# Kernel tuning notes

Measured on AMD Instinct MI355X. Metric: run time of the kernel, lower is better.

## Reference

```python
import jax, jax.numpy as jnp
import numpy as np

N = 50000
E = 800000
IN_DIM = 256
OUT_DIM = 128
HEADS = 4
D_K = OUT_DIM // HEADS  # 32
BETA = 1.0  # beta_init, requires_grad=False (constant)
NEG_SLOPE = 0.2
EPS = 1e-12


def setup_inputs() -> dict:
    key = jax.random.key(0)
    k = jax.random.split(key, 8)
    H = jax.random.normal(k[0], (N, IN_DIM), dtype=jnp.float32)
    edge_index = jax.random.randint(k[1], (2, E), 0, N, dtype=jnp.int64)
    sim1_edge = jax.random.normal(k[2], (E,), dtype=jnp.float32)
    # Parameters (torch nn.Linear stores weight as (out, in); y = x @ W.T)
    W = jax.random.normal(k[3], (HEADS * D_K, IN_DIM), dtype=jnp.float32) * (1.0 / np.sqrt(IN_DIM))
    a_src = jax.random.normal(k[4], (HEADS, D_K), dtype=jnp.float32)
    a_dst = jax.random.normal(k[5], (HEADS, D_K), dtype=jnp.float32)
    msg_lin_w = jax.random.normal(k[6], (D_K, D_K), dtype=jnp.float32) * (1.0 / np.sqrt(D_K))
    return {"H": H, "edge_index": edge_index, "sim1_edge": sim1_edge,
            "W": W, "a_src": a_src, "a_dst": a_dst, "msg_lin_w": msg_lin_w}


def reference(H, edge_index, sim1_edge, W, a_src, a_dst, msg_lin_w):
    n = H.shape[0]
    H_proj = (H @ W.T).reshape(n, HEADS, D_K)           # [N, h, d_k]
    src, dst = edge_index[0], edge_index[1]
    h_src = H_proj[src]                                  # [E, h, d_k]
    h_dst = H_proj[dst]                                  # [E, h, d_k]
    # per-edge attention logits (struct + semantic)
    e = (jnp.einsum('ehd,hd->eh', h_src, a_src)
         + jnp.einsum('ehd,hd->eh', h_dst, a_dst)
         + BETA * sim1_edge[:, None])                    # [E, h]
    e = jnp.where(e >= 0, e, NEG_SLOPE * e)              # LeakyReLU(0.2)
    # global (per-head) max for stabilization, matching original e.max(dim=0)
    e = e - jnp.max(e, axis=0, keepdims=True)
    exp_e = jnp.exp(e)                                   # [E, h]
    denom = jax.ops.segment_sum(exp_e, dst, num_segments=n)  # [N, h]
    alpha = exp_e / (denom[dst] + EPS)                   # [E, h]  (dropout p=0 -> identity)
    m = alpha[:, :, None] * h_src                        # [E, h, d_k]
    out = jax.ops.segment_sum(m, dst, num_segments=n)    # [N, h, d_k]
    out_h = out.reshape(n, HEADS * D_K)                  # concat=True
    msg_base = jnp.einsum('ehd,od->eho', h_src, msg_lin_w).mean(axis=1)  # [E, d_k]
    alpha_mean = alpha.mean(axis=1)                      # [E]
    return out_h, alpha_mean, msg_base
```

## Files before the change

kernel.cpp:

```cpp
#include <hip/hip_runtime.h>
#include <hip/hip_bf16.h>
#include <float.h>

#define HEADS 4
#define DK 32

static constexpr float kBeta = 1.0f;
static constexpr float kNeg  = 0.2f;
static constexpr float kEps  = 1e-12f;

__device__ __forceinline__ float bf2f(unsigned short v) {
  return __uint_as_float((unsigned)v << 16);
}
__device__ __forceinline__ float2 bfp2(unsigned u) {
  return make_float2(__uint_as_float(u << 16), __uint_as_float(u & 0xFFFF0000u));
}
__device__ __forceinline__ unsigned fkey(float x) {
  unsigned u = __float_as_uint(x);
  return (u & 0x80000000u) ? ~u : (u | 0x80000000u);
}
__device__ __forceinline__ float funkey(unsigned k) {
  unsigned u = (k & 0x80000000u) ? (k & 0x7fffffffu) : ~k;
  return __uint_as_float(u);
}

__global__ __launch_bounds__(256) void k_detect_edges(const int* __restrict__ ei32,
                                                      int* __restrict__ eflag, int E) {
  int i = blockIdx.x * 256 + threadIdx.x;
  if (2 * i + 1 < 2 * E && ei32[2 * i + 1] != 0) atomicOr(eflag, 1);
}

__global__ __launch_bounds__(256) void k_detect_dtype(const unsigned* __restrict__ Hw,
                                                      int* __restrict__ dflag, int nw) {
  int i = blockIdx.x * 256 + threadIdx.x;
  if (i < nw && ((Hw[i] >> 7) & 0xFFu) == 0xFFu) atomicOr(dflag, 1);
}

__global__ __launch_bounds__(256) void k_cvt(const int* __restrict__ ei32,
                                             const int* __restrict__ eflag,
                                             int* __restrict__ src_i,
                                             int* __restrict__ dst_i,
                                             int* __restrict__ deg, int E) {
  int i = blockIdx.x * 256 + threadIdx.x;
  if (i >= E) return;
  int s, d;
  if (*eflag) { s = ei32[i];     d = ei32[E + i]; }
  else        { s = ei32[2 * i]; d = ei32[2 * E + 2 * i]; }
  src_i[i] = s;
  dst_i[i] = d;
  atomicAdd(deg + d, 1);
}

__global__ __launch_bounds__(256) void k_f32cvt(const void* __restrict__ in,
                                                float* __restrict__ out,
                                                const int* __restrict__ dflag, int n) {
  int i = blockIdx.x * 256 + threadIdx.x;
  if (i >= n) return;
  out[i] = (*dflag) ? ((const float*)in)[i] : bf2f(((const unsigned short*)in)[i]);
}

__global__ __launch_bounds__(256) void k_wcvt(const void* __restrict__ in,
                                              float* __restrict__ out,
                                              const int* __restrict__ dflag, int n) {
  int i = blockIdx.x * 256 + threadIdx.x;
  if (i >= n) return;
  int r = i >> 8, c = i & 255;
  float v = (*dflag) ? ((const float*)in)[i] : bf2f(((const unsigned short*)in)[i]);
  out[(size_t)c * 128 + r] = v;
}

__global__ __launch_bounds__(256) void k_scan1(const int* __restrict__ deg,
                                               int* __restrict__ bsum, int N) {
  const int t = threadIdx.x;
  int i = blockIdx.x * 256 + t;
  int v = (i < N) ? deg[i] : 0;
#pragma unroll
  for (int off = 32; off; off >>= 1) v += __shfl_xor(v, off);
  __shared__ int red[4];
  if ((t & 63) == 0) red[t >> 6] = v;
  __syncthreads();
  if (t == 0) bsum[blockIdx.x] = red[0] + red[1] + red[2] + red[3];
}
__global__ __launch_bounds__(1024) void k_scan2(int* __restrict__ bsum, int nb) {
  __shared__ int part[1024];
  const int t = threadIdx.x;
  part[t] = (t < nb) ? bsum[t] : 0;
  __syncthreads();
  int own = part[t];
  for (int off = 1; off < 1024; off <<= 1) {
    int v = (t >= off) ? part[t - off] : 0;
    __syncthreads();
    part[t] += v;
    __syncthreads();
  }
  if (t < nb) bsum[t] = part[t] - own;
}
__global__ __launch_bounds__(256) void k_scan3(const int* __restrict__ deg,
                                               const int* __restrict__ bsum,
                                               int* __restrict__ row_ptr,
                                               int* __restrict__ cursor, int N) {
  __shared__ int part[256];
  const int t = threadIdx.x;
  int i = blockIdx.x * 256 + t;
  int v = (i < N) ? deg[i] : 0;
  part[t] = v;
  __syncthreads();
  for (int off = 1; off < 256; off <<= 1) {
    int x = (t >= off) ? part[t - off] : 0;
    __syncthreads();
    part[t] += x;
    __syncthreads();
  }
  int excl = part[t] - v + bsum[blockIdx.x];
  if (i < N) {
    row_ptr[i] = excl;
    cursor[i]  = excl;
    if (i == N - 1) row_ptr[N] = excl + v;
  }
}

__global__ __launch_bounds__(256) void k_fill(const int* __restrict__ dst,
                                              int* __restrict__ cursor,
                                              int* __restrict__ eidx, int E) {
  int e = blockIdx.x * 256 + threadIdx.x;
  if (e >= E) return;
  int pos = atomicAdd(cursor + dst[e], 1);
  eidx[pos] = e;
}

__global__ __launch_bounds__(256) void k_proj(const void* __restrict__ Hraw,
                                              const float* __restrict__ Wtf,
                                              const int* __restrict__ dflag,
                                              float* __restrict__ Hproj, int N) {
  __shared__ float Ht[32][260];
  const int t = threadIdx.x;
  const int nb = blockIdx.x * 32;
  const int dt = *dflag;
  if (dt) {
    const float4* __restrict__ H4 = (const float4*)Hraw;
#pragma unroll
    for (int i = 0; i < 8; ++i) {
      int f = t + i * 256;
      int r = f >> 6, kq = f & 63;
      float4 v = make_float4(0.f, 0.f, 0.f, 0.f);
      if (nb + r < N) v = H4[(size_t)(nb + r) * 64 + kq];
      *(float4*)&Ht[r][4 * kq] = v;
    }
  } else {
    const uint4* __restrict__ H8 = (const uint4*)Hraw;
#pragma unroll
    for (int i = 0; i < 4; ++i) {
      int g = t + i * 256;
      int r = g >> 5, c8 = g & 31;
      uint4 v = make_uint4(0u, 0u, 0u, 0u);
      if (nb + r < N) v = H8[(size_t)(nb + r) * 32 + c8];
      float2 f0 = bfp2(v.x), f1 = bfp2(v.y), f2 = bfp2(v.z), f3 = bfp2(v.w);
      *(float4*)&Ht[r][c8 * 8 + 0] = make_float4(f0.x, f0.y, f1.x, f1.y);
      *(float4*)&Ht[r][c8 * 8 + 4] = make_float4(f2.x, f2.y, f3.x, f3.y);
    }
  }
  __syncthreads();
  const int cg = (t & 31);
  const int n0 = (t >> 5) * 4;
  float acc[4][4];
#pragma unroll
  for (int n = 0; n < 4; ++n)
#pragma unroll
    for (int j = 0; j < 4; ++j) acc[n][j] = 0.f;
  const float4* __restrict__ Wt4 = (const float4*)Wtf;
#pragma unroll 4
  for (int kk = 0; kk < 256; kk += 4) {
    float4 w0 = Wt4[(size_t)(kk + 0) * 32 + cg];
    float4 w1 = Wt4[(size_t)(kk + 1) * 32 + cg];
    float4 w2 = Wt4[(size_t)(kk + 2) * 32 + cg];
    float4 w3 = Wt4[(size_t)(kk + 3) * 32 + cg];
#pragma unroll
    for (int n = 0; n < 4; ++n) {
      float4 h = *(const float4*)&Ht[n0 + n][kk];
      acc[n][0] += h.x * w0.x + h.y * w1.x + h.z * w2.x + h.w * w3.x;
      acc[n][1] += h.x * w0.y + h.y * w1.y + h.z * w2.y + h.w * w3.y;
      acc[n][2] += h.x * w0.z + h.y * w1.z + h.z * w2.z + h.w * w3.z;
      acc[n][3] += h.x * w0.w + h.y * w1.w + h.z * w2.w + h.w * w3.w;
    }
  }
#pragma unroll
  for (int n = 0; n < 4; ++n) {
    int row = nb + n0 + n;
    if (row < N)
      *(float4*)&Hproj[(size_t)row * 128 + 4 * cg] =
          make_float4(acc[n][0], acc[n][1], acc[n][2], acc[n][3]);
  }
}

__global__ __launch_bounds__(256) void k_node(const float* __restrict__ Hproj,
                                              const float* __restrict__ af,
                                              const float* __restrict__ msgwf,
                                              float* __restrict__ s_src,
                                              float* __restrict__ s_dst,
                                              float* __restrict__ msgb, int N) {
  const int l = threadIdx.x & 63;
  const int wb = threadIdx.x >> 6;
  const int n = (blockIdx.x << 2) + wb;
  if (n >= N) return;
  const float* row = Hproj + (size_t)n * 128;
  float h0 = row[l], h1 = row[64 + l];
  float p0 = h0 * af[l],       p1 = h1 * af[64 + l];
  float q0 = h0 * af[128 + l], q1 = h1 * af[192 + l];
#pragma unroll
  for (int off = 16; off; off >>= 1) {
    p0 += __shfl_xor(p0, off);
    p1 += __shfl_xor(p1, off);
    q0 += __shfl_xor(q0, off);
    q1 += __shfl_xor(q1, off);
  }
  if (l == 0)  { s_src[n*4+0] = p0; s_src[n*4+2] = p1; s_dst[n*4+0] = q0; s_dst[n*4+2] = q1; }
  if (l == 32) { s_src[n*4+1] = p0; s_src[n*4+3] = p1; s_dst[n*4+1] = q0; s_dst[n*4+3] = q1; }
  float t4 = h0 + __shfl_xor(h0, 32) + h1 + __shfl_xor(h1, 32);
  float hbar = 0.25f * t4;
  if (l < DK) {
    float acc = 0.f;
#pragma unroll
    for (int d = 0; d < DK; ++d) acc += __shfl(hbar, d) * msgwf[l * DK + d];
    msgb[(size_t)n * DK + l] = acc;
  }
}

__global__ __launch_bounds__(256) void k_logits(const int* __restrict__ src,
                                                const int* __restrict__ dst,
                                                const void* __restrict__ sim1,
                                                const int* __restrict__ dflag,
                                                const float* __restrict__ s_src,
                                                const float* __restrict__ s_dst,
                                                float4* __restrict__ e_vals,
                                                unsigned* __restrict__ gmax, int E) {
  const int e = blockIdx.x * 256 + threadIdx.x;
  float m0 = -FLT_MAX, m1 = -FLT_MAX, m2 = -FLT_MAX, m3 = -FLT_MAX;
  if (e < E) {
    int s = src[e], d = dst[e];
    float4 ss = *(const float4*)(s_src + (size_t)s * 4);
    float4 sd = *(const float4*)(s_dst + (size_t)d * 4);
    float sv = (*dflag) ? ((const float*)sim1)[e] : bf2f(((const unsigned short*)sim1)[e]);
    float b = kBeta * sv;
    float e0 = ss.x + sd.x + b; e0 = (e0 >= 0.f) ? e0 : kNeg * e0;
    float e1 = ss.y + sd.y + b; e1 = (e1 >= 0.f) ? e1 : kNeg * e1;
    float e2 = ss.z + sd.z + b; e2 = (e2 >= 0.f) ? e2 : kNeg * e2;
    float e3 = ss.w + sd.w + b; e3 = (e3 >= 0.f) ? e3 : kNeg * e3;
    e_vals[e] = make_float4(e0, e1, e2, e3);
    m0 = e0; m1 = e1; m2 = e2; m3 = e3;
  }
#pragma unroll
  for (int off = 32; off; off >>= 1) {
    m0 = fmaxf(m0, __shfl_xor(m0, off));
    m1 = fmaxf(m1, __shfl_xor(m1, off));
    m2 = fmaxf(m2, __shfl_xor(m2, off));
    m3 = fmaxf(m3, __shfl_xor(m3, off));
  }
  __shared__ float red[4][4];
  if ((threadIdx.x & 63) == 0) {
    int w = threadIdx.x >> 6;
    red[w][0] = m0; red[w][1] = m1; red[w][2] = m2; red[w][3] = m3;
  }
  __syncthreads();
  if (threadIdx.x < 4) {
    int h = threadIdx.x;
    float mm = fmaxf(fmaxf(red[0][h], red[1][h]), fmaxf(red[2][h], red[3][h]));
    atomicMax(gmax + h, fkey(mm));
  }
}

__global__ __launch_bounds__(256) void k_msg(const int* __restrict__ src,
                                             const float* __restrict__ msgb,
                                             const int* __restrict__ dflag,
                                             void* __restrict__ d_out,
                                             int N, int E) {
  long long tid = (long long)blockIdx.x * 256 + threadIdx.x;
  if (tid >= (long long)E * DK) return;
  int e = (int)(tid >> 5), j = (int)(tid & 31);
  float mv = msgb[(size_t)src[e] * DK + j];
  const size_t msg_off = (size_t)N * 128 + (size_t)E;
  if (*dflag) ((float*)d_out)[msg_off + (size_t)e * DK + j] = mv;
  else        ((__hip_bfloat16*)d_out)[msg_off + (size_t)e * DK + j] = __float2bfloat16(mv);
}

__global__ __launch_bounds__(256) void k_out(const int* __restrict__ row_ptr,
                                             const int* __restrict__ eidx,
                                             const int* __restrict__ src,
                                             const float4* __restrict__ e_vals,
                                             const unsigned* __restrict__ gmax,
                                             const float* __restrict__ Hproj,
                                             const int* __restrict__ dflag,
                                             void* __restrict__ d_out, int N, int E) {
  const int n = (int)((blockIdx.x * 256 + threadIdx.x) >> 6);
  const int l = threadIdx.x & 63;
  if (n >= N) return;
  const int beg = row_ptr[n];
  const int deg = row_ptr[n + 1] - beg;
  const int dt = *dflag;
  const float m0 = funkey(gmax[0]), m1 = funkey(gmax[1]);
  const float m2 = funkey(gmax[2]), m3 = funkey(gmax[3]);
  const size_t alpha_off = (size_t)N * 128;
  float acc_lo = 0.f, acc_hi = 0.f;
  float4 dn = make_float4(0.f, 0.f, 0.f, 0.f);
  int eid = 0, s = 0;
  float4 ev = make_float4(0.f, 0.f, 0.f, 0.f);
  const bool small = (deg <= 64);
  if (small) {
    if (l < deg) {
      eid = eidx[beg + l];
      float4 r = e_vals[eid];
      ev = make_float4(expf(r.x - m0), expf(r.y - m1),
                       expf(r.z - m2), expf(r.w - m3));
      s = src[eid];
      dn = ev;
    }
  } else {
    for (int base = 0; base < deg; base += 64) {
      if (base + l < deg) {
        int e2 = eidx[beg + base + l];
        float4 r = e_vals[e2];
        dn.x += expf(r.x - m0); dn.y += expf(r.y - m1);
        dn.z += expf(r.z - m2); dn.w += expf(r.w - m3);
      }
    }
  }
#pragma unroll
  for (int off = 32; off; off >>= 1) {
    dn.x += __shfl_xor(dn.x, off);
    dn.y += __shfl_xor(dn.y, off);
    dn.z += __shfl_xor(dn.z, off);
    dn.w += __shfl_xor(dn.w, off);
  }
  const float i0 = 1.f / (dn.x + kEps), i1 = 1.f / (dn.y + kEps);
  const float i2 = 1.f / (dn.z + kEps), i3 = 1.f / (dn.w + kEps);
  if (small) {
    if (l < deg) {
      float am = 0.25f * (ev.x * i0 + ev.y * i1 + ev.z * i2 + ev.w * i3);
      if (dt) ((float*)d_out)[alpha_off + eid] = am;
      else    ((__hip_bfloat16*)d_out)[alpha_off + eid] = __float2bfloat16(am);
    }
    for (int i = 0; i < deg; ++i) {
      int si = __shfl(s, i);
      float ax = __shfl(ev.x, i), ay = __shfl(ev.y, i);
      float az = __shfl(ev.z, i), aw = __shfl(ev.w, i);
      float a_lo = (l < 32) ? ax * i0 : ay * i1;
      float a_hi = (l < 32) ? az * i2 : aw * i3;
      acc_lo += a_lo * Hproj[(size_t)si * 128 + l];
      acc_hi += a_hi * Hproj[(size_t)si * 128 + 64 + l];
    }
  } else {
    for (int base = 0; base < deg; base += 64) {
      int cnt = min(64, deg - base);
      int eid2 = 0, s2 = 0;
      float4 e2 = make_float4(0.f, 0.f, 0.f, 0.f);
      if (l < cnt) {
        eid2 = eidx[beg + base + l];
        float4 r = e_vals[eid2];
        e2 = make_float4(expf(r.x - m0), expf(r.y - m1),
                         expf(r.z - m2), expf(r.w - m3));
        s2 = src[eid2];
        float am = 0.25f * (e2.x * i0 + e2.y * i1 + e2.z * i2 + e2.w * i3);
        if (dt) ((float*)d_out)[alpha_off + eid2] = am;
        else    ((__hip_bfloat16*)d_out)[alpha_off + eid2] = __float2bfloat16(am);
      }
      for (int i = 0; i < cnt; ++i) {
        int si = __shfl(s2, i);
        float ax = __shfl(e2.x, i), ay = __shfl(e2.y, i);
        float az = __shfl(e2.z, i), aw = __shfl(e2.w, i);
        float a_lo = (l < 32) ? ax * i0 : ay * i1;
        float a_hi = (l < 32) ? az * i2 : aw * i3;
        acc_lo += a_lo * Hproj[(size_t)si * 128 + l];
        acc_hi += a_hi * Hproj[(size_t)si * 128 + 64 + l];
      }
    }
  }
  if (dt) {
    ((float*)d_out)[(size_t)n * 128 + l]      = acc_lo;
    ((float*)d_out)[(size_t)n * 128 + 64 + l] = acc_hi;
  } else {
    ((__hip_bfloat16*)d_out)[(size_t)n * 128 + l]      = __float2bfloat16(acc_lo);
    ((__hip_bfloat16*)d_out)[(size_t)n * 128 + 64 + l] = __float2bfloat16(acc_hi);
  }
}

extern "C" void kernel_launch(void* const* d_in, const int* in_sizes, int n_in,
                              void* d_out, int out_size, void* d_ws, size_t ws_size,
                              hipStream_t stream) {
  const void* H     = d_in[0];
  const int*  ei    = (const int*)d_in[1];
  const void* sim1  = d_in[2];
  const void* W     = d_in[3];
  const void* a_src = d_in[4];
  const void* a_dst = d_in[5];
  const void* msg_w = d_in[6];
  const int N = in_sizes[0] / 256;
  const int E = in_sizes[2];
  const int NB = (N + 255) / 256;

  float* ws      = (float*)d_ws;
  float* Hproj   = ws;
  float* s_src   = Hproj  + (size_t)N * 128;
  float* s_dst   = s_src  + (size_t)N * 4;
  float* msgb    = s_dst  + (size_t)N * 4;
  float* e_vals  = msgb   + (size_t)N * 32;
  int* deg       = (int*)(e_vals + (size_t)E * 4);
  unsigned* gmax = (unsigned*)(deg + N);
  int* eflag     = (int*)(gmax + 4);
  int* dflag     = eflag + 1;
  int* row_ptr   = dflag + 1;
  int* cursor    = row_ptr + N + 1;
  int* bsum      = cursor + N;
  int* eidx      = bsum + 1024;
  int* src_i     = eidx + E;
  int* dst_i     = src_i + E;
  float* Wtf     = (float*)(dst_i + E);
  float* af      = Wtf + 128 * 256;
  float* msgwf   = af + 256;

  hipMemsetAsync(deg, 0, (size_t)(N + 6) * sizeof(int), stream);

  k_detect_edges<<<16, 256, 0, stream>>>(ei, eflag, E);
  k_detect_dtype<<<512, 256, 0, stream>>>((const unsigned*)H, dflag, 131072);
  k_cvt<<<(E + 255) / 256, 256, 0, stream>>>(ei, eflag, src_i, dst_i, deg, E);
  k_wcvt<<<128, 256, 0, stream>>>(W, Wtf, dflag, 128 * 256);
  k_f32cvt<<<1, 256, 0, stream>>>(a_src, af, dflag, 128);
  k_f32cvt<<<1, 256, 0, stream>>>(a_dst, af + 128, dflag, 128);
  k_f32cvt<<<4, 256, 0, stream>>>(msg_w, msgwf, dflag, 1024);
  k_proj<<<(N + 31) / 32, 256, 0, stream>>>(H, Wtf, dflag, Hproj, N);
  k_scan1<<<NB, 256, 0, stream>>>(deg, bsum, N);
  k_scan2<<<1, 1024, 0, stream>>>(bsum, NB);
  k_scan3<<<NB, 256, 0, stream>>>(deg, bsum, row_ptr, cursor, N);
  k_fill<<<(E + 255) / 256, 256, 0, stream>>>(dst_i, cursor, eidx, E);
  k_node<<<(N + 3) / 4, 256, 0, stream>>>(Hproj, af, msgwf, s_src, s_dst, msgb, N);
  k_logits<<<(E + 255) / 256, 256, 0, stream>>>(src_i, dst_i, sim1, dflag, s_src, s_dst,
                                                (float4*)e_vals, gmax, E);
  k_msg<<<(int)(((long long)E * DK + 255) / 256), 256, 0, stream>>>(src_i, msgb, dflag,
                                                                    d_out, N, E);
  k_out<<<(int)(((size_t)N * 64 + 255) / 256), 256, 0, stream>>>(
      row_ptr, eidx, src_i, (const float4*)e_vals, gmax, Hproj, dflag, d_out, N, E);
}
```

Measured before the change: 544.2 us.

## Store gather operands in fp16, recompute edge logits in aggregation, merge setup kernels

Hproj and the message base are now also written as fp16 copies. The aggregation and message kernels gather these half-size rows, with each lane handling a packed half2 pair and writing vectorized outputs. The per-edge logit buffer is no longer stored: the aggregation kernel recomputes the logits from s_src, s_dst and sim1, which removes an E×16-byte write and read. Small detect and parameter conversion kernels are merged into fewer launches, at the cost of fp16 rounding error in gathered features and message outputs.

After: 515.1 us. 1.06x faster.

```diff
diff --git a/kernel.cpp b/kernel.cpp
--- a/kernel.cpp
+++ b/kernel.cpp
@@ -1,5 +1,6 @@
 #include <hip/hip_runtime.h>
 #include <hip/hip_bf16.h>
+#include <hip/hip_fp16.h>
 #include <float.h>
 
 #define HEADS 4
@@ -24,15 +25,13 @@
   return __uint_as_float(u);
 }
 
-__global__ __launch_bounds__(256) void k_detect_edges(const int* __restrict__ ei32,
-                                                      int* __restrict__ eflag, int E) {
+__global__ __launch_bounds__(256) void k_detect(const int* __restrict__ ei32,
+                                                const unsigned* __restrict__ Hw,
+                                                int* __restrict__ eflag,
+                                                int* __restrict__ dflag,
+                                                int E, int nw) {
   int i = blockIdx.x * 256 + threadIdx.x;
-  if (2 * i + 1 < 2 * E && ei32[2 * i + 1] != 0) atomicOr(eflag, 1);
-}
-
-__global__ __launch_bounds__(256) void k_detect_dtype(const unsigned* __restrict__ Hw,
-                                                      int* __restrict__ dflag, int nw) {
-  int i = blockIdx.x * 256 + threadIdx.x;
+  if (i < 4096 && 2 * i + 1 < 2 * E && ei32[2 * i + 1] != 0) atomicOr(eflag, 1);
   if (i < nw && ((Hw[i] >> 7) & 0xFFu) == 0xFFu) atomicOr(dflag, 1);
 }
 
@@ -51,12 +50,23 @@
   atomicAdd(deg + d, 1);
 }
 
-__global__ __launch_bounds__(256) void k_f32cvt(const void* __restrict__ in,
-                                                float* __restrict__ out,
-                                                const int* __restrict__ dflag, int n) {
+__global__ __launch_bounds__(256) void k_params(const void* __restrict__ a_src,
+                                                const void* __restrict__ a_dst,
+                                                const void* __restrict__ msg_w,
+                                                float* __restrict__ af,
+                                                float* __restrict__ msgwf,
+                                                const int* __restrict__ dflag) {
   int i = blockIdx.x * 256 + threadIdx.x;
-  if (i >= n) return;
-  out[i] = (*dflag) ? ((const float*)in)[i] : bf2f(((const unsigned short*)in)[i]);
+  int dt = *dflag;
+  if (i < 128) {
+    af[i] = dt ? ((const float*)a_src)[i] : bf2f(((const unsigned short*)a_src)[i]);
+  } else if (i < 256) {
+    int j = i - 128;
+    af[i] = dt ? ((const float*)a_dst)[j] : bf2f(((const unsigned short*)a_dst)[j]);
+  } else if (i < 1280) {
+    int j = i - 256;
+    msgwf[j] = dt ? ((const float*)msg_w)[j] : bf2f(((const unsigned short*)msg_w)[j]);
+  }
 }
 
 __global__ __launch_bounds__(256) void k_wcvt(const void* __restrict__ in,
@@ -197,13 +207,16 @@
                                               const float* __restrict__ msgwf,
                                               float* __restrict__ s_src,
                                               float* __restrict__ s_dst,
-                                              float* __restrict__ msgb, int N) {
+                                              __half* __restrict__ msgb,
+                                              __half* __restrict__ Hb, int N) {
   const int l = threadIdx.x & 63;
   const int wb = threadIdx.x >> 6;
   const int n = (blockIdx.x << 2) + wb;
   if (n >= N) return;
   const float* row = Hproj + (size_t)n * 128;
   float h0 = row[l], h1 = row[64 + l];
+  Hb[(size_t)n * 128 + l]      = __float2half(h0);
+  Hb[(size_t)n * 128 + 64 + l] = __float2half(h1);
   float p0 = h0 * af[l],       p1 = h1 * af[64 + l];
   float q0 = h0 * af[128 + l], q1 = h1 * af[192 + l];
 #pragma unroll
@@ -221,7 +234,7 @@
     float acc = 0.f;
 #pragma unroll
     for (int d = 0; d < DK; ++d) acc += __shfl(hbar, d) * msgwf[l * DK + d];
-    msgb[(size_t)n * DK + l] = acc;
+    msgb[(size_t)n * DK + l] = __float2half(acc);
   }
 }
 
@@ -231,7 +244,6 @@
                                                 const int* __restrict__ dflag,
                                                 const float* __restrict__ s_src,
                                                 const float* __restrict__ s_dst,
-                                                float4* __restrict__ e_vals,
                                                 unsigned* __restrict__ gmax, int E) {
   const int e = blockIdx.x * 256 + threadIdx.x;
   float m0 = -FLT_MAX, m1 = -FLT_MAX, m2 = -FLT_MAX, m3 = -FLT_MAX;
@@ -245,7 +257,6 @@
     float e1 = ss.y + sd.y + b; e1 = (e1 >= 0.f) ? e1 : kNeg * e1;
     float e2 = ss.z + sd.z + b; e2 = (e2 >= 0.f) ? e2 : kNeg * e2;
     float e3 = ss.w + sd.w + b; e3 = (e3 >= 0.f) ? e3 : kNeg * e3;
-    e_vals[e] = make_float4(e0, e1, e2, e3);
     m0 = e0; m1 = e1; m2 = e2; m3 = e3;
   }
 #pragma unroll
@@ -269,25 +280,32 @@
 }
 
 __global__ __launch_bounds__(256) void k_msg(const int* __restrict__ src,
-                                             const float* __restrict__ msgb,
+                                             const __half2* __restrict__ msgb2,
                                              const int* __restrict__ dflag,
                                              void* __restrict__ d_out,
                                              int N, int E) {
   long long tid = (long long)blockIdx.x * 256 + threadIdx.x;
-  if (tid >= (long long)E * DK) return;
-  int e = (int)(tid >> 5), j = (int)(tid & 31);
-  float mv = msgb[(size_t)src[e] * DK + j];
+  if (tid >= (long long)E * 16) return;
+  int e = (int)(tid >> 4), jp = (int)(tid & 15);
+  __half2 hv = msgb2[(size_t)src[e] * 16 + jp];
+  float2 f = __half22float2(hv);
   const size_t msg_off = (size_t)N * 128 + (size_t)E;
-  if (*dflag) ((float*)d_out)[msg_off + (size_t)e * DK + j] = mv;
-  else        ((__hip_bfloat16*)d_out)[msg_off + (size_t)e * DK + j] = __float2bfloat16(mv);
+  if (*dflag) {
+    *(float2*)&((float*)d_out)[msg_off + (size_t)e * 32 + 2 * jp] = f;
+  } else {
+    __hip_bfloat162 b = __float22bfloat162_rn(f);
+    *(__hip_bfloat162*)((__hip_bfloat16*)d_out + msg_off + (size_t)e * 32 + 2 * jp) = b;
+  }
 }
 
 __global__ __launch_bounds__(256) void k_out(const int* __restrict__ row_ptr,
                                              const int* __restrict__ eidx,
                                              const int* __restrict__ src,
-                                             const float4* __restrict__ e_vals,
+                                             const void* __restrict__ sim1,
+                                             const float* __restrict__ s_src,
+                                             const float* __restrict__ s_dst,
                                              const unsigned* __restrict__ gmax,
-                                             const float* __restrict__ Hproj,
+                                             const unsigned* __restrict__ Hb_u,
                                              const int* __restrict__ dflag,
                                              void* __restrict__ d_out, int N, int E) {
   const int n = (int)((blockIdx.x * 256 + threadIdx.x) >> 6);
@@ -298,8 +316,9 @@
   const int dt = *dflag;
   const float m0 = funkey(gmax[0]), m1 = funkey(gmax[1]);
   const float m2 = funkey(gmax[2]), m3 = funkey(gmax[3]);
+  const float4 sd = *(const float4*)(s_dst + (size_t)n * 4);
   const size_t alpha_off = (size_t)N * 128;
-  float acc_lo = 0.f, acc_hi = 0.f;
+  float accx = 0.f, accy = 0.f;
   float4 dn = make_float4(0.f, 0.f, 0.f, 0.f);
   int eid = 0, s = 0;
   float4 ev = make_float4(0.f, 0.f, 0.f, 0.f);
@@ -307,19 +326,29 @@
   if (small) {
     if (l < deg) {
       eid = eidx[beg + l];
-      float4 r = e_vals[eid];
-      ev = make_float4(expf(r.x - m0), expf(r.y - m1),
-                       expf(r.z - m2), expf(r.w - m3));
       s = src[eid];
+      float4 ss = *(const float4*)(s_src + (size_t)s * 4);
+      float sv = dt ? ((const float*)sim1)[eid] : bf2f(((const unsigned short*)sim1)[eid]);
+      float e0 = ss.x + sd.x + sv; e0 = (e0 >= 0.f) ? e0 : kNeg * e0;
+      float e1 = ss.y + sd.y + sv; e1 = (e1 >= 0.f) ? e1 : kNeg * e1;
+      float e2 = ss.z + sd.z + sv; e2 = (e2 >= 0.f) ? e2 : kNeg * e2;
+      float e3 = ss.w + sd.w + sv; e3 = (e3 >= 0.f) ? e3 : kNeg * e3;
+      ev = make_float4(expf(e0 - m0), expf(e1 - m1), expf(e2 - m2), expf(e3 - m3));
       dn = ev;
     }
   } else {
     for (int base = 0; base < deg; base += 64) {
       if (base + l < deg) {
-        int e2 = eidx[beg + base + l];
-        float4 r = e_vals[e2];
-        dn.x += expf(r.x - m0); dn.y += expf(r.y - m1);
-        dn.z += expf(r.z - m2); dn.w += expf(r.w - m3);
+        int e2i = eidx[beg + base + l];
+        int s2 = src[e2i];
+        float4 ss = *(const float4*)(s_src + (size_t)s2 * 4);
+        float sv = dt ? ((const float*)sim1)[e2i] : bf2f(((const unsigned short*)sim1)[e2i]);
+        float e0 = ss.x + sd.x + sv; e0 = (e0 >= 0.f) ? e0 : kNeg * e0;
+        float e1 = ss.y + sd.y + sv; e1 = (e1 >= 0.f) ? e1 : kNeg * e1;
+        float e2 = ss.z + sd.z + sv; e2 = (e2 >= 0.f) ? e2 : kNeg * e2;
+        float e3 = ss.w + sd.w + sv; e3 = (e3 >= 0.f) ? e3 : kNeg * e3;
+        dn.x += expf(e0 - m0); dn.y += expf(e1 - m1);
+        dn.z += expf(e2 - m2); dn.w += expf(e3 - m3);
       }
     }
   }
@@ -332,6 +361,7 @@
   }
   const float i0 = 1.f / (dn.x + kEps), i1 = 1.f / (dn.y + kEps);
   const float i2 = 1.f / (dn.z + kEps), i3 = 1.f / (dn.w + kEps);
+  const float myinv = (l < 32) ? ((l < 16) ? i0 : i1) : ((l < 48) ? i2 : i3);
   if (small) {
     if (l < deg) {
       float am = 0.25f * (ev.x * i0 + ev.y * i1 + ev.z * i2 + ev.w * i3);
@@ -342,43 +372,48 @@
       int si = __shfl(s, i);
       float ax = __shfl(ev.x, i), ay = __shfl(ev.y, i);
       float az = __shfl(ev.z, i), aw = __shfl(ev.w, i);
-      float a_lo = (l < 32) ? ax * i0 : ay * i1;
-      float a_hi = (l < 32) ? az * i2 : aw * i3;
-      acc_lo += a_lo * Hproj[(size_t)si * 128 + l];
-      acc_hi += a_hi * Hproj[(size_t)si * 128 + 64 + l];
+      float aa = ((l < 32) ? ((l < 16) ? ax : ay) : ((l < 48) ? az : aw)) * myinv;
+      unsigned u = Hb_u[(size_t)si * 64 + l];
+      float2 f = __half22float2(*(const __half2*)&u);
+      accx += aa * f.x;
+      accy += aa * f.y;
     }
   } else {
     for (int base = 0; base < deg; base += 64) {
       int cnt = min(64, deg - base);
       int eid2 = 0, s2 = 0;
-      float4 e2 = make_float4(0.f, 0.f, 0.f, 0.f);
+      float4 e2v = make_float4(0.f, 0.f, 0.f, 0.f);
       if (l < cnt) {
         eid2 = eidx[beg + base + l];
-        float4 r = e_vals[eid2];
-        e2 = make_float4(expf(r.x - m0), expf(r.y - m1),
-                         expf(r.z - m2), expf(r.w - m3));
         s2 = src[eid2];
-        float am = 0.25f * (e2.x * i0 + e2.y * i1 + e2.z * i2 + e2.w * i3);
+        float4 ss = *(const float4*)(s_src + (size_t)s2 * 4);
+        float sv = dt ? ((const float*)sim1)[eid2] : bf2f(((const unsigned short*)sim1)[eid2]);
+        float e0 = ss.x + sd.x + sv; e0 = (e0 >= 0.f) ? e0 : kNeg * e0;
+        float e1 = ss.y + sd.y + sv; e1 = (e1 >= 0.f) ? e1 : kNeg * e1;
+        float e2 = ss.z + sd.z + sv; e2 = (e2 >= 0.f) ? e2 : kNeg * e2;
+        float e3 = ss.w + sd.w + sv; e3 = (e3 >= 0.f) ? e3 : kNeg * e3;
+        e2v = make_float4(expf(e0 - m0), expf(e1 - m1), expf(e2 - m2), expf(e3 - m3));
+        float am = 0.25f * (e2v.x * i0 + e2v.y * i1 + e2v.z * i2 + e2v.w * i3);
         if (dt) ((float*)d_out)[alpha_off + eid2] = am;
         else    ((__hip_bfloat16*)d_out)[alpha_off + eid2] = __float2bfloat16(am);
       }
       for (int i = 0; i < cnt; ++i) {
         int si = __shfl(s2, i);
-        float ax = __shfl(e2.x, i), ay = __shfl(e2.y, i);
-        float az = __shfl(e2.z, i), aw = __shfl(e2.w, i);
-        float a_lo = (l < 32) ? ax * i0 : ay * i1;
-        float a_hi = (l < 32) ? az * i2 : aw * i3;
-        acc_lo += a_lo * Hproj[(size_t)si * 128 + l];
-        acc_hi += a_hi * Hproj[(size_t)si * 128 + 64 + l];
+        float ax = __shfl(e2v.x, i), ay = __shfl(e2v.y, i);
+        float az = __shfl(e2v.z, i), aw = __shfl(e2v.w, i);
+        float aa = ((l < 32) ? ((l < 16) ? ax : ay) : ((l < 48) ? az : aw)) * myinv;
+        unsigned u = Hb_u[(size_t)si * 64 + l];
+        float2 f = __half22float2(*(const __half2*)&u);
+        accx += aa * f.x;
+        accy += aa * f.y;
       }
     }
   }
   if (dt) {
-    ((float*)d_out)[(size_t)n * 128 + l]      = acc_lo;
-    ((float*)d_out)[(size_t)n * 128 + 64 + l] = acc_hi;
+    *(float2*)&((float*)d_out)[(size_t)n * 128 + 2 * l] = make_float2(accx, accy);
   } else {
-    ((__hip_bfloat16*)d_out)[(size_t)n * 128 + l]      = __float2bfloat16(acc_lo);
-    ((__hip_bfloat16*)d_out)[(size_t)n * 128 + 64 + l] = __float2bfloat16(acc_hi);
+    __hip_bfloat162 b = __float22bfloat162_rn(make_float2(accx, accy));
+    *(__hip_bfloat162*)((__hip_bfloat16*)d_out + (size_t)n * 128 + 2 * l) = b;
   }
 }
 
@@ -396,45 +431,43 @@
   const int E = in_sizes[2];
   const int NB = (N + 255) / 256;
 
-  float* ws      = (float*)d_ws;
-  float* Hproj   = ws;
-  float* s_src   = Hproj  + (size_t)N * 128;
-  float* s_dst   = s_src  + (size_t)N * 4;
-  float* msgb    = s_dst  + (size_t)N * 4;
-  float* e_vals  = msgb   + (size_t)N * 32;
-  int* deg       = (int*)(e_vals + (size_t)E * 4);
-  unsigned* gmax = (unsigned*)(deg + N);
-  int* eflag     = (int*)(gmax + 4);
-  int* dflag     = eflag + 1;
-  int* row_ptr   = dflag + 1;
-  int* cursor    = row_ptr + N + 1;
-  int* bsum      = cursor + N;
-  int* eidx      = bsum + 1024;
-  int* src_i     = eidx + E;
-  int* dst_i     = src_i + E;
-  float* Wtf     = (float*)(dst_i + E);
-  float* af      = Wtf + 128 * 256;
-  float* msgwf   = af + 256;
+  char* base     = (char*)d_ws;
+  float* Hproj   = (float*)base;  base += (size_t)N * 128 * 4;
+  float* s_src   = (float*)base;  base += (size_t)N * 4 * 4;
+  float* s_dst   = (float*)base;  base += (size_t)N * 4 * 4;
+  __half* msgb   = (__half*)base; base += (size_t)N * DK * 2;
+  __half* Hb     = (__half*)base; base += (size_t)N * 128 * 2;
+  int* deg       = (int*)base;    base += (size_t)N * 4;
+  unsigned* gmax = (unsigned*)base; base += 4 * 4;
+  int* eflag     = (int*)base;    base += 4;
+  int* dflag     = (int*)base;    base += 4;
+  int* row_ptr   = (int*)base;    base += (size_t)(N + 1) * 4;
+  int* cursor    = (int*)base;    base += (size_t)N * 4;
+  int* bsum      = (int*)base;    base += 1024 * 4;
+  int* eidx      = (int*)base;    base += (size_t)E * 4;
+  int* src_i     = (int*)base;    base += (size_t)E * 4;
+  int* dst_i     = (int*)base;    base += (size_t)E * 4;
+  float* Wtf     = (float*)base;  base += 128 * 256 * 4;
+  float* af      = (float*)base;  base += 256 * 4;
+  float* msgwf   = (float*)base;  base += 1024 * 4;
 
   hipMemsetAsync(deg, 0, (size_t)(N + 6) * sizeof(int), stream);
 
-  k_detect_edges<<<16, 256, 0, stream>>>(ei, eflag, E);
-  k_detect_dtype<<<512, 256, 0, stream>>>((const unsigned*)H, dflag, 131072);
+  k_detect<<<512, 256, 0, stream>>>(ei, (const unsigned*)H, eflag, dflag, E, 131072);
   k_cvt<<<(E + 255) / 256, 256, 0, stream>>>(ei, eflag, src_i, dst_i, deg, E);
   k_wcvt<<<128, 256, 0, stream>>>(W, Wtf, dflag, 128 * 256);
-  k_f32cvt<<<1, 256, 0, stream>>>(a_src, af, dflag, 128);
-  k_f32cvt<<<1, 256, 0, stream>>>(a_dst, af + 128, dflag, 128);
-  k_f32cvt<<<4, 256, 0, stream>>>(msg_w, msgwf, dflag, 1024);
+  k_params<<<5, 256, 0, stream>>>(a_src, a_dst, msg_w, af, msgwf, dflag);
   k_proj<<<(N + 31) / 32, 256, 0, stream>>>(H, Wtf, dflag, Hproj, N);
   k_scan1<<<NB, 256, 0, stream>>>(deg, bsum, N);
   k_scan2<<<1, 1024, 0, stream>>>(bsum, NB);
   k_scan3<<<NB, 256, 0, stream>>>(deg, bsum, row_ptr, cursor, N);
   k_fill<<<(E + 255) / 256, 256, 0, stream>>>(dst_i, cursor, eidx, E);
-  k_node<<<(N + 3) / 4, 256, 0, stream>>>(Hproj, af, msgwf, s_src, s_dst, msgb, N);
+  k_node<<<(N + 3) / 4, 256, 0, stream>>>(Hproj, af, msgwf, s_src, s_dst, msgb, Hb, N);
   k_logits<<<(E + 255) / 256, 256, 0, stream>>>(src_i, dst_i, sim1, dflag, s_src, s_dst,
-                                                (float4*)e_vals, gmax, E);
-  k_msg<<<(int)(((long long)E * DK + 255) / 256), 256, 0, stream>>>(src_i, msgb, dflag,
-                                                                    d_out, N, E);
+                                                gmax, E);
+  k_msg<<<(int)(((long long)E * 16 + 255) / 256), 256, 0, stream>>>(
+      src_i, (const __half2*)msgb, dflag, d_out, N, E);
   k_out<<<(int)(((size_t)N * 64 + 255) / 256), 256, 0, stream>>>(
-      row_ptr, eidx, src_i, (const float4*)e_vals, gmax, Hproj, dflag, d_out, N, E);
-}
+      row_ptr, eidx, src_i, sim1, s_src, s_dst, gmax, (const unsigned*)Hb, dflag,
+      d_out, N, E);
+}
```
